# Kernel tuning notes

Hardware: AMD Instinct MI355X
Metric: run time of the kernel (lower is better)

## Reference

```python
import jax, jax.numpy as jnp
import numpy as np

BATCH = 8
N_POINTS = 2048
HOP = 1  # hop_length


def setup_inputs() -> dict:
    key = jax.random.key(0)
    kx = jax.random.fold_in(key, 0)
    x = jax.random.normal(kx, (BATCH, N_POINTS), dtype=jnp.float32)
    # learnable window-width parameter (init_lambd = 20.0)
    lambd = jnp.full((1,), 20.0, dtype=jnp.float32)
    return {"x": x, "lambd": lambd}


def reference(x, lambd):
    """Batched differentiable Gaussian-window spectrogram.

    Equivalent to looping over the batch and calling
    tf.differentiable_spectrogram(x[i] - mean(x[i]), |lambd|, hop_length=HOP):
    a Gaussian window over the WHOLE signal centered at t_c = 0, HOP, ..., n,
    followed by a zero-padded one-sided FFT (n_fft = 2n) and power spectrum.
    Output: (B, 1, n+1, n//HOP + 1).
    """
    B, n = x.shape
    sigma = jnp.abs(lambd)[0]
    # per-sample mean subtraction
    x = x - jnp.mean(x, axis=1, keepdims=True)
    t = jnp.arange(n, dtype=jnp.float32)                       # (n,)
    t_c = jnp.arange(0, n + 1, HOP, dtype=jnp.float32)         # (F,) frame centers
    # Gaussian windows over the whole signal, one per frame center: (F, n)
    windows = jnp.exp(-0.5 * jnp.square((t[None, :] - t_c[:, None]) / sigma))
    # windowed signals: (B, F, n)
    xw = x[:, None, :] * windows[None, :, :]
    # zero-padded one-sided FFT -> n+1 frequency bins: (B, F, n+1)
    spec = jnp.fft.rfft(xw, n=2 * n, axis=-1)
    power = spec.real ** 2 + spec.imag ** 2                    # power spectrogram
    # (B, 1, n+1 freq, F time)
    return jnp.swapaxes(power, 1, 2)[:, None, :, :]
```

## Files before the change

kernel.cpp:

```cpp
#include <hip/hip_runtime.h>
#include <math.h>

#define NPTS    2048
#define NBINS   2049
#define NFRAMES 2049
#define U       192
#define PAD     96
#define XPLEN   2560

#define MTOT    4224
#define MBLK    33
#define NBLK    9
#define BM      128
#define BN      256
#define BK      64
#define SPAN    (BN + U)
#define SSTRIDE 464
#define ASTRIDE 72
#define ABUF    (BM * ASTRIDE)

typedef __attribute__((ext_vector_type(8))) short short8_t;
typedef __attribute__((ext_vector_type(4))) short short4_t;
typedef __attribute__((ext_vector_type(4))) float float4_t;

static __device__ __forceinline__ unsigned short f2bf(float f) {
    unsigned u = __float_as_uint(f);
    unsigned r = (u + 0x7fffu + ((u >> 16) & 1u)) >> 16;
    return (unsigned short)r;
}

__global__ void prep_kernel(const float* __restrict__ x, unsigned short* __restrict__ xp) {
    __shared__ float red[256];
    const int b = blockIdx.x;
    float s = 0.f;
    for (int t = threadIdx.x; t < NPTS; t += 256) s += x[b * NPTS + t];
    red[threadIdx.x] = s;
    __syncthreads();
    for (int off = 128; off > 0; off >>= 1) {
        if (threadIdx.x < off) red[threadIdx.x] += red[threadIdx.x + off];
        __syncthreads();
    }
    const float mean = red[0] * (1.f / (float)NPTS);
    for (int t = threadIdx.x; t < XPLEN; t += 256) {
        const int s2 = t - PAD;
        float v = (s2 >= 0 && s2 < NPTS) ? (x[b * NPTS + s2] - mean) : 0.f;
        xp[b * XPLEN + t] = f2bf(v);
    }
}

#define WCH 3
__global__ void wgen_kernel(const float* __restrict__ lambd, unsigned short* __restrict__ W) {
    const int idx = blockIdx.x * 256 + threadIdx.x;
    if (idx >= MTOT * WCH) return;
    const int m  = idx / WCH;
    const int ch = idx - m * WCH;
    const int k = m >> 1, p = m & 1;
    unsigned int* wp = (unsigned int*)(W + (size_t)m * U + ch * 64);
    if (k >= NBINS) {
        #pragma unroll
        for (int j = 0; j < 32; ++j) wp[j] = 0u;
        return;
    }
    const float sigma  = fabsf(lambd[0]);
    const float inv2s2 = 0.5f / (sigma * sigma);
    const float u0 = (float)(ch * 64 - PAD);
    const float dphi = (float)M_PI * (float)k * (1.f / 2048.f);
    float sn, cs, sd, cd;
    sincosf(dphi * u0, &sn, &cs);
    sincosf(dphi, &sd, &cd);
    float       g  = __expf(-u0 * u0 * inv2s2);
    float       gr = __expf(-(2.f * u0 + 1.f) * inv2s2);
    const float gq = __expf(-2.f * inv2s2);
    #pragma unroll
    for (int j = 0; j < 32; ++j) {
        unsigned short lo = f2bf(g * (p ? sn : cs));
        float cn = cs * cd - sn * sd; sn = fmaf(sn, cd, cs * sd); cs = cn;
        g *= gr; gr *= gq;
        unsigned short hi = f2bf(g * (p ? sn : cs));
        cn = cs * cd - sn * sd; sn = fmaf(sn, cd, cs * sd); cs = cn;
        g *= gr; gr *= gq;
        wp[j] = (unsigned int)lo | ((unsigned int)hi << 16);
    }
}

__global__ __launch_bounds__(256, 2) void spec_mfma(
        const unsigned short* __restrict__ W, const unsigned short* __restrict__ xp,
        float* __restrict__ out) {
    __shared__ unsigned short Alds[2 * ABUF];
    __shared__ unsigned short span[4 * SSTRIDE];

    const int tid = threadIdx.x;
    const int b  = blockIdx.z;
    const int n0 = blockIdx.x * BN;
    const int m0 = blockIdx.y * BM;

    {
        const unsigned short* xpb = xp + b * XPLEN;
        for (int i = tid; i < 4 * SPAN; i += 256) {
            const int c = i / SPAN;
            const int t = i - c * SPAN;
            span[c * SSTRIDE + t] = xpb[n0 + t + c];
        }
    }

    const int lane = tid & 63;
    const int wv   = tid >> 6;
    const int wm   = (wv & 1) * 64;
    const int wn   = (wv >> 1) * 128;
    const int col  = lane & 15;
    const int q    = lane >> 4;

    const int row  = tid >> 1;
    const int half = tid & 1;
    const unsigned short* wrow = W + (size_t)(m0 + row) * U + half * 32;
    const int lbase = row * ASTRIDE + half * 32;

    const int cc = col & 3;
    const unsigned short* bbase = span + cc * SSTRIDE + (wn + col - cc) + 8 * q;

    float4_t acc[4][8];
    #pragma unroll
    for (int mt = 0; mt < 4; ++mt)
        #pragma unroll
        for (int nt = 0; nt < 8; ++nt)
            acc[mt][nt] = (float4_t){0.f, 0.f, 0.f, 0.f};

    float4 r0, r1, r2, r3;
    {
        const float4* g4 = (const float4*)(wrow);
        r0 = g4[0]; r1 = g4[1]; r2 = g4[2]; r3 = g4[3];
        float4* l4 = (float4*)(Alds + lbase);
        l4[0] = r0; l4[1] = r1; l4[2] = r2; l4[3] = r3;
        const float4* g5 = (const float4*)(wrow + BK);
        r0 = g5[0]; r1 = g5[1]; r2 = g5[2]; r3 = g5[3];
    }
    __syncthreads();

    #pragma unroll
    for (int s = 0; s < 3; ++s) {
        if (s < 2) {
            float4* l4 = (float4*)(Alds + ((s + 1) & 1) * ABUF + lbase);
            l4[0] = r0; l4[1] = r1; l4[2] = r2; l4[3] = r3;
        }
        if (s < 1) {
            const float4* g4 = (const float4*)(wrow + (s + 2) * BK);
            r0 = g4[0]; r1 = g4[1]; r2 = g4[2]; r3 = g4[3];
        }
        const unsigned short* cur = Alds + (s & 1) * ABUF;
        const int kb = s * BK;
        #pragma unroll
        for (int ks = 0; ks < 2; ++ks) {
            const int kk = ks * 32;
            short8_t af[4], bf[8];
            #pragma unroll
            for (int mt = 0; mt < 4; ++mt)
                af[mt] = *(const short8_t*)(cur + (wm + mt * 16 + col) * ASTRIDE + kk + q * 8);
            #pragma unroll
            for (int nt = 0; nt < 8; ++nt) {
                const unsigned short* p = bbase + nt * 16 + kb + kk;
                short4_t lo = *(const short4_t*)(p);
                short4_t hi = *(const short4_t*)(p + 4);
                bf[nt] = __builtin_shufflevector(lo, hi, 0, 1, 2, 3, 4, 5, 6, 7);
            }
            #pragma unroll
            for (int mt = 0; mt < 4; ++mt)
                #pragma unroll
                for (int nt = 0; nt < 8; ++nt)
                    acc[mt][nt] = __builtin_amdgcn_mfma_f32_16x16x32_bf16(
                        af[mt], bf[nt], acc[mt][nt], 0, 0, 0);
        }
        __syncthreads();
    }

    const int fbase = n0 + wn + col;
    #pragma unroll
    for (int mt = 0; mt < 4; ++mt) {
        const int mrow = m0 + wm + mt * 16 + q * 4;
        const int kk0  = mrow >> 1;
        #pragma unroll
        for (int nt = 0; nt < 8; ++nt) {
            const int f = fbase + nt * 16;
            if (f < NFRAMES) {
                const float4_t a = acc[mt][nt];
                const float p0 = a[0] * a[0] + a[1] * a[1];
                const float p1 = a[2] * a[2] + a[3] * a[3];
                if (kk0 < NBINS)
                    out[((size_t)b * NBINS + kk0) * NFRAMES + f] = p0;
                if (kk0 + 1 < NBINS)
                    out[((size_t)b * NBINS + kk0 + 1) * NFRAMES + f] = p1;
            }
        }
    }
}

extern "C" void kernel_launch(void* const* d_in, const int* in_sizes, int n_in,
                              void* d_out, int out_size, void* d_ws, size_t ws_size,
                              hipStream_t stream) {
    const float* x     = (const float*)d_in[0];
    const float* lambd = (const float*)d_in[1];
    float*       out   = (float*)d_out;

    char* ws = (char*)d_ws;
    unsigned short* xp = (unsigned short*)ws;
    unsigned short* W  = (unsigned short*)(ws + 43264);

    hipLaunchKernelGGL(prep_kernel, dim3(8), dim3(256), 0, stream, x, xp);
    hipLaunchKernelGGL(wgen_kernel, dim3((MTOT * WCH + 255) / 256), dim3(256), 0, stream,
                       lambd, W);

    dim3 grid(NBLK, MBLK, 8);
    hipLaunchKernelGGL(spec_mfma, grid, dim3(256), 0, stream, W, xp, out);
}
```

Baseline: 175.0 us.

## Reuse Toeplitz B fragments across k-steps and merge prep with window generation

Keeps 8 shifted copies of the signal span in LDS so each lane can load B fragments as aligned 16-byte reads. It exploits the Toeplitz structure: a fragment for tile nt at k-step j is the same as the one for tile nt+2j, so each k-step rotates a register ring and loads only two new fragments. The mean-subtraction and window-generation kernels are merged into one launch, and window generation now uses finer chunks with fast sincos and exact modular phase reduction. The trade is more LDS, more live registers and slightly lower-precision trig.

```diff
diff --git a/kernel.cpp b/kernel.cpp
--- a/kernel.cpp
+++ b/kernel.cpp
@@ -16,11 +16,11 @@
 #define BK      64
 #define SPAN    (BN + U)
 #define SSTRIDE 464
+#define NCOPY   8
 #define ASTRIDE 72
 #define ABUF    (BM * ASTRIDE)
 
 typedef __attribute__((ext_vector_type(8))) short short8_t;
-typedef __attribute__((ext_vector_type(4))) short short4_t;
 typedef __attribute__((ext_vector_type(4))) float float4_t;
 
 static __device__ __forceinline__ unsigned short f2bf(float f) {
@@ -29,50 +29,53 @@
     return (unsigned short)r;
 }
 
-__global__ void prep_kernel(const float* __restrict__ x, unsigned short* __restrict__ xp) {
-    __shared__ float red[256];
-    const int b = blockIdx.x;
-    float s = 0.f;
-    for (int t = threadIdx.x; t < NPTS; t += 256) s += x[b * NPTS + t];
-    red[threadIdx.x] = s;
-    __syncthreads();
-    for (int off = 128; off > 0; off >>= 1) {
-        if (threadIdx.x < off) red[threadIdx.x] += red[threadIdx.x + off];
+#define WCH 6
+#define WGBLK ((MTOT * WCH + 255) / 256)
+__global__ void prep_kernel(const float* __restrict__ x, const float* __restrict__ lambd,
+                            unsigned short* __restrict__ xp, unsigned short* __restrict__ W) {
+    if (blockIdx.x < 8) {
+        __shared__ float red[256];
+        const int b = blockIdx.x;
+        float s = 0.f;
+        for (int t = threadIdx.x; t < NPTS; t += 256) s += x[b * NPTS + t];
+        red[threadIdx.x] = s;
         __syncthreads();
-    }
-    const float mean = red[0] * (1.f / (float)NPTS);
-    for (int t = threadIdx.x; t < XPLEN; t += 256) {
-        const int s2 = t - PAD;
-        float v = (s2 >= 0 && s2 < NPTS) ? (x[b * NPTS + s2] - mean) : 0.f;
-        xp[b * XPLEN + t] = f2bf(v);
-    }
-}
-
-#define WCH 3
-__global__ void wgen_kernel(const float* __restrict__ lambd, unsigned short* __restrict__ W) {
-    const int idx = blockIdx.x * 256 + threadIdx.x;
+        for (int off = 128; off > 0; off >>= 1) {
+            if (threadIdx.x < off) red[threadIdx.x] += red[threadIdx.x + off];
+            __syncthreads();
+        }
+        const float mean = red[0] * (1.f / (float)NPTS);
+        for (int t = threadIdx.x; t < XPLEN; t += 256) {
+            const int s2 = t - PAD;
+            float v = (s2 >= 0 && s2 < NPTS) ? (x[b * NPTS + s2] - mean) : 0.f;
+            xp[b * XPLEN + t] = f2bf(v);
+        }
+        return;
+    }
+    const int idx = (blockIdx.x - 8) * 256 + threadIdx.x;
     if (idx >= MTOT * WCH) return;
     const int m  = idx / WCH;
     const int ch = idx - m * WCH;
     const int k = m >> 1, p = m & 1;
-    unsigned int* wp = (unsigned int*)(W + (size_t)m * U + ch * 64);
+    unsigned int* wp = (unsigned int*)(W + (size_t)m * U + ch * 32);
     if (k >= NBINS) {
         #pragma unroll
-        for (int j = 0; j < 32; ++j) wp[j] = 0u;
+        for (int j = 0; j < 16; ++j) wp[j] = 0u;
         return;
     }
     const float sigma  = fabsf(lambd[0]);
     const float inv2s2 = 0.5f / (sigma * sigma);
-    const float u0 = (float)(ch * 64 - PAD);
-    const float dphi = (float)M_PI * (float)k * (1.f / 2048.f);
+    const int   u0i = ch * 32 - PAD;
+    const float u0  = (float)u0i;
+    const float TWO_PI = 6.28318530717958647692f;
     float sn, cs, sd, cd;
-    sincosf(dphi * u0, &sn, &cs);
-    sincosf(dphi, &sd, &cd);
+    __sincosf(TWO_PI * (1.f / 4096.f) * (float)((k * u0i) & 4095), &sn, &cs);
+    __sincosf(TWO_PI * (1.f / 4096.f) * (float)k, &sd, &cd);
     float       g  = __expf(-u0 * u0 * inv2s2);
     float       gr = __expf(-(2.f * u0 + 1.f) * inv2s2);
     const float gq = __expf(-2.f * inv2s2);
     #pragma unroll
-    for (int j = 0; j < 32; ++j) {
+    for (int j = 0; j < 16; ++j) {
         unsigned short lo = f2bf(g * (p ? sn : cs));
         float cn = cs * cd - sn * sd; sn = fmaf(sn, cd, cs * sd); cs = cn;
         g *= gr; gr *= gq;
@@ -87,7 +90,7 @@
         const unsigned short* __restrict__ W, const unsigned short* __restrict__ xp,
         float* __restrict__ out) {
     __shared__ unsigned short Alds[2 * ABUF];
-    __shared__ unsigned short span[4 * SSTRIDE];
+    __shared__ unsigned short span[NCOPY * SSTRIDE];
 
     const int tid = threadIdx.x;
     const int b  = blockIdx.z;
@@ -96,7 +99,7 @@
 
     {
         const unsigned short* xpb = xp + b * XPLEN;
-        for (int i = tid; i < 4 * SPAN; i += 256) {
+        for (int i = tid; i < NCOPY * SPAN; i += 256) {
             const int c = i / SPAN;
             const int t = i - c * SPAN;
             span[c * SSTRIDE + t] = xpb[n0 + t + c];
@@ -115,7 +118,7 @@
     const unsigned short* wrow = W + (size_t)(m0 + row) * U + half * 32;
     const int lbase = row * ASTRIDE + half * 32;
 
-    const int cc = col & 3;
+    const int cc = col & 7;
     const unsigned short* bbase = span + cc * SSTRIDE + (wn + col - cc) + 8 * q;
 
     float4_t acc[4][8];
@@ -136,6 +139,11 @@
     }
     __syncthreads();
 
+    short8_t bf[8];
+    #pragma unroll
+    for (int d = 0; d < 8; ++d)
+        bf[d] = *(const short8_t*)(bbase + 16 * d);
+
     #pragma unroll
     for (int s = 0; s < 3; ++s) {
         if (s < 2) {
@@ -147,27 +155,29 @@
             r0 = g4[0]; r1 = g4[1]; r2 = g4[2]; r3 = g4[3];
         }
         const unsigned short* cur = Alds + (s & 1) * ABUF;
-        const int kb = s * BK;
         #pragma unroll
         for (int ks = 0; ks < 2; ++ks) {
+            const int j  = s * 2 + ks;
             const int kk = ks * 32;
-            short8_t af[4], bf[8];
+            short8_t af[4];
             #pragma unroll
             for (int mt = 0; mt < 4; ++mt)
                 af[mt] = *(const short8_t*)(cur + (wm + mt * 16 + col) * ASTRIDE + kk + q * 8);
-            #pragma unroll
-            for (int nt = 0; nt < 8; ++nt) {
-                const unsigned short* p = bbase + nt * 16 + kb + kk;
-                short4_t lo = *(const short4_t*)(p);
-                short4_t hi = *(const short4_t*)(p + 4);
-                bf[nt] = __builtin_shufflevector(lo, hi, 0, 1, 2, 3, 4, 5, 6, 7);
+            short8_t nb0, nb1;
+            if (j < 5) {
+                nb0 = *(const short8_t*)(bbase + 16 * (2 * j + 8));
+                nb1 = *(const short8_t*)(bbase + 16 * (2 * j + 9));
             }
             #pragma unroll
             for (int mt = 0; mt < 4; ++mt)
                 #pragma unroll
                 for (int nt = 0; nt < 8; ++nt)
                     acc[mt][nt] = __builtin_amdgcn_mfma_f32_16x16x32_bf16(
-                        af[mt], bf[nt], acc[mt][nt], 0, 0, 0);
+                        af[mt], bf[(nt + 2 * j) & 7], acc[mt][nt], 0, 0, 0);
+            if (j < 5) {
+                bf[(2 * j) & 7]     = nb0;
+                bf[(2 * j + 1) & 7] = nb1;
+            }
         }
         __syncthreads();
     }
@@ -204,9 +214,7 @@
     unsigned short* xp = (unsigned short*)ws;
     unsigned short* W  = (unsigned short*)(ws + 43264);
 
-    hipLaunchKernelGGL(prep_kernel, dim3(8), dim3(256), 0, stream, x, xp);
-    hipLaunchKernelGGL(wgen_kernel, dim3((MTOT * WCH + 255) / 256), dim3(256), 0, stream,
-                       lambd, W);
+    hipLaunchKernelGGL(prep_kernel, dim3(8 + WGBLK), dim3(256), 0, stream, x, lambd, xp, W);
 
     dim3 grid(NBLK, MBLK, 8);
     hipLaunchKernelGGL(spec_mfma, grid, dim3(256), 0, stream, W, xp, out);
```

Result: no change. 172.1 us (-1.7%).
